# Kernel tuning notes

Hardware: AMD Instinct MI355X
Metric: run time of the kernel (lower is better)

## Reference

```python
import jax, jax.numpy as jnp
import numpy as np

D = 1024  # input_size == context_size
B, SQ, SKV = 4, 2048, 2048


def setup_inputs() -> dict:
    key = jax.random.key(0)
    ks = jax.random.split(key, 8)
    s = 1.0 / np.sqrt(D)
    return {
        "x": jax.random.normal(ks[0], (B, SQ, D), jnp.float32),
        "context": jax.random.normal(ks[1], (B, SKV, D), jnp.float32),
        "Wq": jax.random.uniform(ks[2], (D, D), jnp.float32, -s, s),
        "bq": jnp.zeros((D,), jnp.float32),
        "Wk": jax.random.uniform(ks[3], (D, D), jnp.float32, -s, s),
        "bk": jnp.zeros((D,), jnp.float32),
        "Wv": jax.random.uniform(ks[4], (D, D), jnp.float32, -s, s),
        "bv": jnp.zeros((D,), jnp.float32),
    }


def reference(x, context, Wq, bq, Wk, bk, Wv, bv):
    # Linear layers (torch nn.Linear: y = x @ W^T + b; here W stored as [in, out])
    Q = x @ Wq + bq                  # [B, SQ, D]
    K = context @ Wk + bk            # [B, SKV, D]
    V = context @ Wv + bv            # [B, SKV, D]
    scale = 1.0 / np.sqrt(D).astype(np.float32)
    scores = jnp.einsum("bqd,bkd->bqk", Q, K) * scale  # [B, SQ, SKV]
    attn = jax.nn.softmax(scores, axis=-1)
    out = jnp.einsum("bqk,bkd->bqd", attn, V)          # [B, SQ, D]
    return out
```

## Files before the change

### kernel.cpp

```cpp
#include <hip/hip_runtime.h>
#include <cstdint>
#include <cstddef>

typedef __attribute__((ext_vector_type(8))) short short8;
typedef __attribute__((ext_vector_type(16))) float floatx16;

__device__ __forceinline__ unsigned short f2bf(float f) {
    union { float f; unsigned int u; } v; v.f = f;
    unsigned int r = v.u + 0x7fffu + ((v.u >> 16) & 1u);
    return (unsigned short)(r >> 16);
}

__device__ __forceinline__ void glds16(const void* g, void* l) {
    __builtin_amdgcn_global_load_lds(
        (const __attribute__((address_space(1))) void*)g,
        (__attribute__((address_space(3))) void*)l, 16, 0, 0);
}

#define EPI_ROW(r, kg) (((r) & 3) + 8 * ((r) >> 2) + 4 * (kg))

__device__ __forceinline__ void gemm_core(
    const unsigned short* __restrict__ Ab, int ldA,
    const unsigned short* __restrict__ Bb, int ldB,
    int K,
    unsigned short* __restrict__ As, unsigned short* __restrict__ Bs,
    floatx16 (&acc)[2][2])
{
    const int tid = threadIdx.x;
    const int wave = tid >> 6, lane = tid & 63;

    const unsigned short* gA[4];
    const unsigned short* gB[4];
#pragma unroll
    for (int i = 0; i < 4; ++i) {
        const int c = i * 256 + tid;
        const int row = c >> 3;
        const int l = (c & 7) ^ ((row ^ (row >> 3)) & 7);
        gA[i] = Ab + (size_t)row * ldA + l * 8;
        gB[i] = Bb + (size_t)row * ldB + l * 8;
    }
    const int arow = (wave >> 1) * 64 + (lane & 31);
    const int brow = (wave & 1) * 64 + (lane & 31);
    const int kg = lane >> 5;
    const int sw = (lane & 7) ^ ((lane >> 3) & 3);
    const unsigned short* pa = As + arow * 64;
    const unsigned short* pb = Bs + brow * 64;

    for (int k0 = 0; k0 < K; k0 += 64) {
#pragma unroll
        for (int i = 0; i < 4; ++i)
            glds16(gA[i] + k0, As + (size_t)(i * 256 + wave * 64) * 8);
#pragma unroll
        for (int i = 0; i < 4; ++i)
            glds16(gB[i] + k0, Bs + (size_t)(i * 256 + wave * 64) * 8);
        __syncthreads();
#pragma unroll
        for (int s = 0; s < 4; ++s) {
            const int o0 = ((2 * s + kg) ^ sw) * 8;
            const int o1 = o0 ^ 32;
            short8 a0 = *(const short8*)(pa + o0);
            short8 a1 = *(const short8*)(pa + 32 * 64 + o1);
            short8 b0 = *(const short8*)(pb + o0);
            short8 b1 = *(const short8*)(pb + 32 * 64 + o1);
            acc[0][0] = __builtin_amdgcn_mfma_f32_32x32x16_bf16(a0, b0, acc[0][0], 0, 0, 0);
            acc[0][1] = __builtin_amdgcn_mfma_f32_32x32x16_bf16(a0, b1, acc[0][1], 0, 0, 0);
            acc[1][0] = __builtin_amdgcn_mfma_f32_32x32x16_bf16(a1, b0, acc[1][0], 0, 0, 0);
            acc[1][1] = __builtin_amdgcn_mfma_f32_32x32x16_bf16(a1, b1, acc[1][1], 0, 0, 0);
        }
        __syncthreads();
    }
}

__global__ __launch_bounds__(256) void prep_kernel(
    const float* __restrict__ x, const float* __restrict__ ctx,
    const float* __restrict__ Wq, const float* __restrict__ Wk, const float* __restrict__ Wv,
    unsigned short* __restrict__ xb, unsigned short* __restrict__ cb,
    unsigned short* __restrict__ Wt0, unsigned short* __restrict__ WtKV,
    float* __restrict__ lrow) {
    const int b = blockIdx.x;
    if (b < 16384) {
        int i = b * 256 + threadIdx.x;
        const float* in; unsigned short* out; int j;
        if (i < 2097152) { in = x; out = xb; j = i; }
        else { in = ctx; out = cb; j = i - 2097152; }
        float4 v = reinterpret_cast<const float4*>(in)[j];
        ushort4 o;
        o.x = f2bf(v.x); o.y = f2bf(v.y); o.z = f2bf(v.z); o.w = f2bf(v.w);
        reinterpret_cast<ushort4*>(out)[j] = o;
    } else if (b < 19456) {
        __shared__ float tile[32][33];
        const int z = b - 16384;
        const int w = z >> 10, t = z & 1023;
        const float* in = (w == 0) ? Wq : (w == 1) ? Wk : Wv;
        unsigned short* out = (w == 0) ? Wt0 : (w == 1) ? WtKV : (WtKV + 1024 * 1024);
        const int c0 = (t & 31) * 32, r0 = (t >> 5) * 32;
        const int tx = threadIdx.x & 31, ty = threadIdx.x >> 5;
#pragma unroll
        for (int j = 0; j < 4; ++j)
            tile[ty + j * 8][tx] = in[(size_t)(r0 + ty + j * 8) * 1024 + c0 + tx];
        __syncthreads();
#pragma unroll
        for (int j = 0; j < 4; ++j)
            out[(size_t)(c0 + ty + j * 8) * 1024 + r0 + tx] = f2bf(tile[tx][ty + j * 8]);
    } else {
        const int i = (b - 19456) * 256 + threadIdx.x;
        reinterpret_cast<float4*>(lrow)[i] = float4{0.f, 0.f, 0.f, 0.f};
    }
}

__global__ __launch_bounds__(256, 4) void qkv_kernel(
    const unsigned short* __restrict__ xb, const unsigned short* __restrict__ cb,
    const unsigned short* __restrict__ WtQ, const unsigned short* __restrict__ WtKV,
    const float* __restrict__ bq, const float* __restrict__ bk, const float* __restrict__ bv,
    unsigned short* __restrict__ Qb, unsigned short* __restrict__ Kb,
    unsigned short* __restrict__ Vt) {
    __shared__ unsigned short As[128 * 64];
    __shared__ unsigned short Bs[128 * 64];
    const int i = blockIdx.x;
    const bool isQ = i < 512;
    int by, bxcol;
    const unsigned short *A, *B;
    if (isQ) {
        const int slot = i >> 3;
        by = (i & 7) + 8 * (slot & 7);
        const int bx = slot >> 3; bxcol = bx * 128;
        A = xb + (size_t)by * 128 * 1024;
        B = WtQ + (size_t)bx * 128 * 1024;
    } else {
        const int j = i - 512;
        const int slot = j >> 3;
        by = (j & 7) + 8 * (slot & 7);
        const int bx = slot >> 3; bxcol = bx * 128;
        A = cb + (size_t)by * 128 * 1024;
        B = WtKV + (size_t)bx * 128 * 1024;
    }
    floatx16 acc[2][2];
#pragma unroll
    for (int a = 0; a < 2; ++a)
#pragma unroll
        for (int bj = 0; bj < 2; ++bj)
#pragma unroll
            for (int r = 0; r < 16; ++r) acc[a][bj][r] = 0.f;

    gemm_core(A, 1024, B, 1024, 1024, As, Bs, acc);

    const int wave = threadIdx.x >> 6, lane = threadIdx.x & 63;
    const int kg = lane >> 5;
    const int cm = by * 128 + (wave >> 1) * 64;
    const int cn = bxcol + (wave & 1) * 64 + (lane & 31);
    if (isQ || bxcol < 1024) {
        unsigned short* O = isQ ? Qb : Kb;
        const float* bias = isQ ? bq : bk;
#pragma unroll
        for (int nt = 0; nt < 2; ++nt) {
            const int col = cn + nt * 32;
            const float bvv = bias[col];
#pragma unroll
            for (int mt = 0; mt < 2; ++mt)
#pragma unroll
                for (int r = 0; r < 16; ++r) {
                    const int row = cm + mt * 32 + EPI_ROW(r, kg);
                    O[(size_t)row * 1024 + col] = f2bf(acc[mt][nt][r] + bvv);
                }
        }
    } else {
#pragma unroll
        for (int nt = 0; nt < 2; ++nt) {
            const int colv = cn + nt * 32 - 1024;
            const float bvv = bv[colv];
#pragma unroll
            for (int mt = 0; mt < 2; ++mt) {
                const int rowg = cm + mt * 32 + 4 * kg;
                const int b = rowg >> 11, qb = rowg & 2047;
#pragma unroll
                for (int g = 0; g < 4; ++g) {
                    const int q = qb + 8 * g;
                    ushort4 u;
                    u.x = f2bf(acc[mt][nt][g * 4 + 0] + bvv);
                    u.y = f2bf(acc[mt][nt][g * 4 + 1] + bvv);
                    u.z = f2bf(acc[mt][nt][g * 4 + 2] + bvv);
                    u.w = f2bf(acc[mt][nt][g * 4 + 3] + bvv);
                    *reinterpret_cast<ushort4*>(Vt + (size_t)b * 2097152 + (size_t)colv * 2048 + q) = u;
                }
            }
        }
    }
}

__global__ __launch_bounds__(256, 4) void qkt_kernel(
    const unsigned short* __restrict__ Qb, const unsigned short* __restrict__ Kb,
    unsigned short* __restrict__ Sb, float* __restrict__ l) {
    __shared__ unsigned short As[128 * 64];
    __shared__ unsigned short Bs[128 * 64];
    const int i = blockIdx.x;
    const int z = (i >> 1) & 3;
    const int slot = i >> 3;
    const int by = (i & 1) + 2 * (slot & 7);
    const int bx = slot >> 3;
    const unsigned short* A = Qb + (size_t)z * 2097152 + (size_t)by * 128 * 1024;
    const unsigned short* B = Kb + (size_t)z * 2097152 + (size_t)bx * 128 * 1024;
    floatx16 acc[2][2];
#pragma unroll
    for (int a = 0; a < 2; ++a)
#pragma unroll
        for (int bj = 0; bj < 2; ++bj)
#pragma unroll
            for (int r = 0; r < 16; ++r) acc[a][bj][r] = 0.f;

    gemm_core(A, 1024, B, 1024, 1024, As, Bs, acc);

    const int wave = threadIdx.x >> 6, lane = threadIdx.x & 63;
    const int kg = lane >> 5;
    unsigned short* C = Sb + (size_t)z * 4194304;
    float* lz = l + z * 2048;
    const int cm = by * 128 + (wave >> 1) * 64;
    const int cn = bx * 128 + (wave & 1) * 64 + (lane & 31);
#pragma unroll
    for (int mt = 0; mt < 2; ++mt)
#pragma unroll
        for (int r = 0; r < 16; ++r) {
            const int row = cm + mt * 32 + EPI_ROW(r, kg);
            const float e0 = __expf(acc[mt][0][r] * 0.03125f);
            const float e1 = __expf(acc[mt][1][r] * 0.03125f);
            C[(size_t)row * 2048 + cn] = f2bf(e0);
            C[(size_t)row * 2048 + cn + 32] = f2bf(e1);
            float s = e0 + e1;
            s += __shfl_xor(s, 1);  s += __shfl_xor(s, 2);
            s += __shfl_xor(s, 4);  s += __shfl_xor(s, 8);
            s += __shfl_xor(s, 16);
            if ((lane & 31) == (mt * 16 + r)) atomicAdd(&lz[row], s);
        }
}

__global__ __launch_bounds__(256, 4) void pv_kernel(
    const unsigned short* __restrict__ Sb, const unsigned short* __restrict__ Vt,
    const float* __restrict__ l, float* __restrict__ out) {
    __shared__ unsigned short As[128 * 64];
    __shared__ unsigned short Bs[128 * 64];
    const int i = blockIdx.x;
    const int z = (i >> 1) & 3;
    const int slot = i >> 3;
    const int by = (i & 1) + 2 * (slot & 7);
    const int bx = slot >> 3;
    const unsigned short* A = Sb + (size_t)z * 4194304 + (size_t)by * 128 * 2048;
    const unsigned short* B = Vt + (size_t)z * 2097152 + (size_t)bx * 128 * 2048;
    floatx16 acc[2][2];
#pragma unroll
    for (int a = 0; a < 2; ++a)
#pragma unroll
        for (int bj = 0; bj < 2; ++bj)
#pragma unroll
            for (int r = 0; r < 16; ++r) acc[a][bj][r] = 0.f;

    gemm_core(A, 2048, B, 2048, 2048, As, Bs, acc);

    const int wave = threadIdx.x >> 6, lane = threadIdx.x & 63;
    const int kg = lane >> 5;
    float* C = out + (size_t)z * 2097152;
    const float* lz = l + z * 2048;
    const int cm = by * 128 + (wave >> 1) * 64;
    const int cn = bx * 128 + (wave & 1) * 64 + (lane & 31);
#pragma unroll
    for (int mt = 0; mt < 2; ++mt)
#pragma unroll
        for (int r = 0; r < 16; ++r) {
            const int row = cm + mt * 32 + EPI_ROW(r, kg);
            const float inv = 1.0f / lz[row];
            C[(size_t)row * 1024 + cn] = acc[mt][0][r] * inv;
            C[(size_t)row * 1024 + cn + 32] = acc[mt][1][r] * inv;
        }
}

extern "C" void kernel_launch(void* const* d_in, const int* in_sizes, int n_in,
                              void* d_out, int out_size, void* d_ws, size_t ws_size,
                              hipStream_t stream) {
    const float* x   = (const float*)d_in[0];
    const float* ctx = (const float*)d_in[1];
    const float* Wq  = (const float*)d_in[2];
    const float* bq  = (const float*)d_in[3];
    const float* Wk  = (const float*)d_in[4];
    const float* bk  = (const float*)d_in[5];
    const float* Wv  = (const float*)d_in[6];
    const float* bv  = (const float*)d_in[7];
    float* out = (float*)d_out;

    const size_t MB = 1024 * 1024;
    char* ws = (char*)d_ws;
    unsigned short* xb   = (unsigned short*)(ws + 0 * MB);
    unsigned short* cb   = (unsigned short*)(ws + 16 * MB);
    unsigned short* Qb   = (unsigned short*)(ws + 32 * MB);
    unsigned short* Kb   = (unsigned short*)(ws + 48 * MB);
    unsigned short* Vt   = (unsigned short*)(ws + 64 * MB);
    unsigned short* Wt0  = (unsigned short*)(ws + 80 * MB);
    unsigned short* WtKV = (unsigned short*)(ws + 82 * MB);
    unsigned short* Sb   = (unsigned short*)(ws + 86 * MB);
    float*          lrow = (float*)(ws + 118 * MB);

    prep_kernel<<<16384 + 3072 + 8, 256, 0, stream>>>(
        x, ctx, Wq, Wk, Wv, xb, cb, Wt0, WtKV, lrow);
    qkv_kernel<<<1536, 256, 0, stream>>>(xb, cb, Wt0, WtKV, bq, bk, bv, Qb, Kb, Vt);
    qkt_kernel<<<1024, 256, 0, stream>>>(Qb, Kb, Sb, lrow);
    pv_kernel<<<512, 256, 0, stream>>>(Sb, Vt, lrow, out);
}
```

Baseline: 271.4 us.

## Fuse QK^T and PV kernels with per-row-block counters for overlap

Merges the score (exp(QK^T)) and PV GEMM kernels into one launch. The first 1024 blocks compute score tiles and bump a per-(batch,row-block) counter with release semantics. The remaining 512 blocks spin on that counter before running the PV GEMM, so PV work can start as soon as its row block is done instead of waiting for a full kernel boundary. It also vectorizes the weight-transpose loads and stores in the prep kernel. The spin-wait depends on block dispatch order and adds atomic and fence overhead.

```diff
diff --git a/kernel.cpp b/kernel.cpp
--- a/kernel.cpp
+++ b/kernel.cpp
@@ -76,7 +76,7 @@
     const float* __restrict__ Wq, const float* __restrict__ Wk, const float* __restrict__ Wv,
     unsigned short* __restrict__ xb, unsigned short* __restrict__ cb,
     unsigned short* __restrict__ Wt0, unsigned short* __restrict__ WtKV,
-    float* __restrict__ lrow) {
+    float* __restrict__ lrow, unsigned int* __restrict__ cnt) {
     const int b = blockIdx.x;
     if (b < 16384) {
         int i = b * 256 + threadIdx.x;
@@ -94,17 +94,21 @@
         const float* in = (w == 0) ? Wq : (w == 1) ? Wk : Wv;
         unsigned short* out = (w == 0) ? Wt0 : (w == 1) ? WtKV : (WtKV + 1024 * 1024);
         const int c0 = (t & 31) * 32, r0 = (t >> 5) * 32;
-        const int tx = threadIdx.x & 31, ty = threadIdx.x >> 5;
-#pragma unroll
-        for (int j = 0; j < 4; ++j)
-            tile[ty + j * 8][tx] = in[(size_t)(r0 + ty + j * 8) * 1024 + c0 + tx];
-        __syncthreads();
-#pragma unroll
-        for (int j = 0; j < 4; ++j)
-            out[(size_t)(c0 + ty + j * 8) * 1024 + r0 + tx] = f2bf(tile[tx][ty + j * 8]);
+        const int tq = threadIdx.x & 7, tr = threadIdx.x >> 3;
+        float4 v = *reinterpret_cast<const float4*>(&in[(size_t)(r0 + tr) * 1024 + c0 + tq * 4]);
+        tile[tr][tq * 4 + 0] = v.x; tile[tr][tq * 4 + 1] = v.y;
+        tile[tr][tq * 4 + 2] = v.z; tile[tr][tq * 4 + 3] = v.w;
+        __syncthreads();
+        ushort4 u;
+        u.x = f2bf(tile[tq * 4 + 0][tr]);
+        u.y = f2bf(tile[tq * 4 + 1][tr]);
+        u.z = f2bf(tile[tq * 4 + 2][tr]);
+        u.w = f2bf(tile[tq * 4 + 3][tr]);
+        *reinterpret_cast<ushort4*>(&out[(size_t)(c0 + tr) * 1024 + r0 + tq * 4]) = u;
     } else {
         const int i = (b - 19456) * 256 + threadIdx.x;
         reinterpret_cast<float4*>(lrow)[i] = float4{0.f, 0.f, 0.f, 0.f};
+        if (b == 19463 && threadIdx.x < 64) cnt[threadIdx.x] = 0u;
     }
 }
 
@@ -187,88 +191,98 @@
     }
 }
 
-__global__ __launch_bounds__(256, 4) void qkt_kernel(
+__global__ __launch_bounds__(256, 4) void qktpv_kernel(
     const unsigned short* __restrict__ Qb, const unsigned short* __restrict__ Kb,
-    unsigned short* __restrict__ Sb, float* __restrict__ l) {
+    const unsigned short* __restrict__ Vt, unsigned short* __restrict__ Sb,
+    float* __restrict__ lrow, unsigned int* __restrict__ cnt,
+    float* __restrict__ out) {
     __shared__ unsigned short As[128 * 64];
     __shared__ unsigned short Bs[128 * 64];
-    const int i = blockIdx.x;
-    const int z = (i >> 1) & 3;
-    const int slot = i >> 3;
-    const int by = (i & 1) + 2 * (slot & 7);
-    const int bx = slot >> 3;
-    const unsigned short* A = Qb + (size_t)z * 2097152 + (size_t)by * 128 * 1024;
-    const unsigned short* B = Kb + (size_t)z * 2097152 + (size_t)bx * 128 * 1024;
-    floatx16 acc[2][2];
-#pragma unroll
-    for (int a = 0; a < 2; ++a)
-#pragma unroll
-        for (int bj = 0; bj < 2; ++bj)
-#pragma unroll
-            for (int r = 0; r < 16; ++r) acc[a][bj][r] = 0.f;
-
-    gemm_core(A, 1024, B, 1024, 1024, As, Bs, acc);
-
-    const int wave = threadIdx.x >> 6, lane = threadIdx.x & 63;
-    const int kg = lane >> 5;
-    unsigned short* C = Sb + (size_t)z * 4194304;
-    float* lz = l + z * 2048;
-    const int cm = by * 128 + (wave >> 1) * 64;
-    const int cn = bx * 128 + (wave & 1) * 64 + (lane & 31);
-#pragma unroll
-    for (int mt = 0; mt < 2; ++mt)
-#pragma unroll
-        for (int r = 0; r < 16; ++r) {
-            const int row = cm + mt * 32 + EPI_ROW(r, kg);
-            const float e0 = __expf(acc[mt][0][r] * 0.03125f);
-            const float e1 = __expf(acc[mt][1][r] * 0.03125f);
-            C[(size_t)row * 2048 + cn] = f2bf(e0);
-            C[(size_t)row * 2048 + cn + 32] = f2bf(e1);
-            float s = e0 + e1;
-            s += __shfl_xor(s, 1);  s += __shfl_xor(s, 2);
-            s += __shfl_xor(s, 4);  s += __shfl_xor(s, 8);
-            s += __shfl_xor(s, 16);
-            if ((lane & 31) == (mt * 16 + r)) atomicAdd(&lz[row], s);
+    const int bid = blockIdx.x;
+
+    if (bid < 1024) {
+        const int g = bid >> 4;
+        const int z = g >> 4, by = g & 15;
+        const int bx = bid & 15;
+        const unsigned short* A = Qb + (size_t)z * 2097152 + (size_t)by * 128 * 1024;
+        const unsigned short* B = Kb + (size_t)z * 2097152 + (size_t)bx * 128 * 1024;
+        floatx16 acc[2][2];
+#pragma unroll
+        for (int a = 0; a < 2; ++a)
+#pragma unroll
+            for (int bj = 0; bj < 2; ++bj)
+#pragma unroll
+                for (int r = 0; r < 16; ++r) acc[a][bj][r] = 0.f;
+
+        gemm_core(A, 1024, B, 1024, 1024, As, Bs, acc);
+
+        const int wave = threadIdx.x >> 6, lane = threadIdx.x & 63;
+        const int kg = lane >> 5;
+        unsigned short* C = Sb + (size_t)z * 4194304;
+        float* lz = lrow + z * 2048;
+        const int cm = by * 128 + (wave >> 1) * 64;
+        const int cn = bx * 128 + (wave & 1) * 64 + (lane & 31);
+#pragma unroll
+        for (int mt = 0; mt < 2; ++mt)
+#pragma unroll
+            for (int r = 0; r < 16; ++r) {
+                const int row = cm + mt * 32 + EPI_ROW(r, kg);
+                const float e0 = __expf(acc[mt][0][r] * 0.03125f);
+                const float e1 = __expf(acc[mt][1][r] * 0.03125f);
+                C[(size_t)row * 2048 + cn] = f2bf(e0);
+                C[(size_t)row * 2048 + cn + 32] = f2bf(e1);
+                float s = e0 + e1;
+                s += __shfl_xor(s, 1);  s += __shfl_xor(s, 2);
+                s += __shfl_xor(s, 4);  s += __shfl_xor(s, 8);
+                s += __shfl_xor(s, 16);
+                if ((lane & 31) == (mt * 16 + r)) atomicAdd(&lz[row], s);
+            }
+        __threadfence();
+        __syncthreads();
+        if (threadIdx.x == 0)
+            __hip_atomic_fetch_add(&cnt[g], 1u,
+                                   __ATOMIC_RELEASE, __HIP_MEMORY_SCOPE_AGENT);
+    } else {
+        const int c = bid - 1024;
+        const int g = c >> 3;
+        const int z = g >> 4, by = g & 15;
+        const int bx = c & 7;
+        if (threadIdx.x == 0) {
+            while (__hip_atomic_load(&cnt[g],
+                                     __ATOMIC_ACQUIRE, __HIP_MEMORY_SCOPE_AGENT) < 16u)
+                __builtin_amdgcn_s_sleep(8);
         }
-}
-
-__global__ __launch_bounds__(256, 4) void pv_kernel(
-    const unsigned short* __restrict__ Sb, const unsigned short* __restrict__ Vt,
-    const float* __restrict__ l, float* __restrict__ out) {
-    __shared__ unsigned short As[128 * 64];
-    __shared__ unsigned short Bs[128 * 64];
-    const int i = blockIdx.x;
-    const int z = (i >> 1) & 3;
-    const int slot = i >> 3;
-    const int by = (i & 1) + 2 * (slot & 7);
-    const int bx = slot >> 3;
-    const unsigned short* A = Sb + (size_t)z * 4194304 + (size_t)by * 128 * 2048;
-    const unsigned short* B = Vt + (size_t)z * 2097152 + (size_t)bx * 128 * 2048;
-    floatx16 acc[2][2];
-#pragma unroll
-    for (int a = 0; a < 2; ++a)
-#pragma unroll
-        for (int bj = 0; bj < 2; ++bj)
-#pragma unroll
-            for (int r = 0; r < 16; ++r) acc[a][bj][r] = 0.f;
-
-    gemm_core(A, 2048, B, 2048, 2048, As, Bs, acc);
-
-    const int wave = threadIdx.x >> 6, lane = threadIdx.x & 63;
-    const int kg = lane >> 5;
-    float* C = out + (size_t)z * 2097152;
-    const float* lz = l + z * 2048;
-    const int cm = by * 128 + (wave >> 1) * 64;
-    const int cn = bx * 128 + (wave & 1) * 64 + (lane & 31);
-#pragma unroll
-    for (int mt = 0; mt < 2; ++mt)
-#pragma unroll
-        for (int r = 0; r < 16; ++r) {
-            const int row = cm + mt * 32 + EPI_ROW(r, kg);
-            const float inv = 1.0f / lz[row];
-            C[(size_t)row * 1024 + cn] = acc[mt][0][r] * inv;
-            C[(size_t)row * 1024 + cn + 32] = acc[mt][1][r] * inv;
-        }
+        __syncthreads();
+        __threadfence();
+
+        const unsigned short* A = Sb + (size_t)z * 4194304 + (size_t)by * 128 * 2048;
+        const unsigned short* B = Vt + (size_t)z * 2097152 + (size_t)bx * 128 * 2048;
+        floatx16 acc[2][2];
+#pragma unroll
+        for (int a = 0; a < 2; ++a)
+#pragma unroll
+            for (int bj = 0; bj < 2; ++bj)
+#pragma unroll
+                for (int r = 0; r < 16; ++r) acc[a][bj][r] = 0.f;
+
+        gemm_core(A, 2048, B, 2048, 2048, As, Bs, acc);
+
+        const int wave = threadIdx.x >> 6, lane = threadIdx.x & 63;
+        const int kg = lane >> 5;
+        float* C = out + (size_t)z * 2097152;
+        const float* lz = lrow + z * 2048;
+        const int cm = by * 128 + (wave >> 1) * 64;
+        const int cn = bx * 128 + (wave & 1) * 64 + (lane & 31);
+#pragma unroll
+        for (int mt = 0; mt < 2; ++mt)
+#pragma unroll
+            for (int r = 0; r < 16; ++r) {
+                const int row = cm + mt * 32 + EPI_ROW(r, kg);
+                const float inv = 1.0f / lz[row];
+                C[(size_t)row * 1024 + cn] = acc[mt][0][r] * inv;
+                C[(size_t)row * 1024 + cn + 32] = acc[mt][1][r] * inv;
+            }
+    }
 }
 
 extern "C" void kernel_launch(void* const* d_in, const int* in_sizes, int n_in,
@@ -295,10 +309,10 @@
     unsigned short* WtKV = (unsigned short*)(ws + 82 * MB);
     unsigned short* Sb   = (unsigned short*)(ws + 86 * MB);
     float*          lrow = (float*)(ws + 118 * MB);
+    unsigned int*   cnt  = (unsigned int*)(ws + 118 * MB + 32768);
 
     prep_kernel<<<16384 + 3072 + 8, 256, 0, stream>>>(
-        x, ctx, Wq, Wk, Wv, xb, cb, Wt0, WtKV, lrow);
+        x, ctx, Wq, Wk, Wv, xb, cb, Wt0, WtKV, lrow, cnt);
     qkv_kernel<<<1536, 256, 0, stream>>>(xb, cb, Wt0, WtKV, bq, bk, bv, Qb, Kb, Vt);
-    qkt_kernel<<<1024, 256, 0, stream>>>(Qb, Kb, Sb, lrow);
-    pv_kernel<<<512, 256, 0, stream>>>(Sb, Vt, lrow, out);
-}
+    qktpv_kernel<<<1536, 256, 0, stream>>>(Qb, Kb, Vt, Sb, lrow, cnt, out);
+}
```

Result: slower. 528.2 us (+94.7%).
